# Performance work log

Measured on AMD Instinct MI355X. Metric: run time of the kernel, lower is better.

The kernel has to match this reference:

```python
import jax, jax.numpy as jnp
import numpy as np

L, B, N, D, H = 18, 2, 1024, 256, 4
DH = D // H  # head_dim = 64
LAYER_TYPES = ("self", "cross") * 9
BN_EPS = 1e-5


def setup_inputs() -> dict:
    key = jax.random.key(0)
    ks = jax.random.split(key, 8)
    s = 0.03  # small init scale keeps 18 residual layers numerically tame
    w = lambda k, shape: jax.random.normal(k, shape, jnp.float32) * s
    return dict(
        descriptors=jax.random.normal(ks[0], (B, 2, N, D), jnp.float32),
        mask=jnp.ones((B, 2, N), jnp.int32),
        qw=w(ks[1], (L, D, D)), qb=jnp.zeros((L, D), jnp.float32),
        kw=w(ks[2], (L, D, D)), kb=jnp.zeros((L, D), jnp.float32),
        vw=w(ks[3], (L, D, D)), vb=jnp.zeros((L, D), jnp.float32),
        ow=w(ks[4], (L, D, D)), ob=jnp.zeros((L, D), jnp.float32),
        w1=w(ks[5], (L, 2 * D, 2 * D)), b1=jnp.zeros((L, 2 * D), jnp.float32),
        bn_g=jnp.ones((L, 2 * D), jnp.float32), bn_b=jnp.zeros((L, 2 * D), jnp.float32),
        w2=w(ks[6], (L, 2 * D, D)), b2=jnp.zeros((L, D), jnp.float32),
    )


def _attention(x, src, m, i, qw, qb, kw, kb, vw, vb, ow, ob):
    b, n, d = x.shape
    q = (x @ qw[i] + qb[i]).reshape(b, n, H, DH)
    k = (src @ kw[i] + kb[i]).reshape(b, -1, H, DH)
    v = (src @ vw[i] + vb[i]).reshape(b, -1, H, DH)
    scores = jnp.einsum("bnhd,bmhd->bhnm", q, k) / (DH ** 0.5)
    scores = jnp.where(m[:, None, None, :] == 0, jnp.float32(-1e9), scores)
    probs = jax.nn.softmax(scores, axis=-1)  # fp32, matches torch dtype=float32
    out = jnp.einsum("bhnm,bmhd->bnhd", probs, v).reshape(b, n, d)
    return out @ ow[i] + ob[i]


def _propagate(x, src, m, i, qw, qb, kw, kb, vw, vb, ow, ob, w1, b1, bn_g, bn_b, w2, b2):
    a = _attention(x, src, m, i, qw, qb, kw, kb, vw, vb, ow, ob)
    h = jnp.concatenate([x, a], axis=-1)        # [B, N, 2D]
    h = h @ w1[i] + b1[i]                       # [B, N, 2D]
    # BatchNorm1d (training mode): per-channel stats over batch and keypoint dims
    mean = h.mean(axis=(0, 1))
    var = ((h - mean) ** 2).mean(axis=(0, 1))   # biased variance, as torch BN uses
    h = (h - mean) / jnp.sqrt(var + BN_EPS) * bn_g[i] + bn_b[i]
    h = jax.nn.relu(h)
    return h @ w2[i] + b2[i]                    # [B, N, D]


def reference(descriptors, mask, qw, qb, kw, kb, vw, vb, ow, ob, w1, b1, bn_g, bn_b, w2, b2):
    d0, d1 = descriptors[:, 0], descriptors[:, 1]
    m0, m1 = mask[:, 0], mask[:, 1]
    params = (qw, qb, kw, kb, vw, vb, ow, ob, w1, b1, bn_g, bn_b, w2, b2)
    for i, lt in enumerate(LAYER_TYPES):
        if lt == "cross":
            s0, s1, sm0, sm1 = d1, d0, m1, m0
        else:  # self
            s0, s1, sm0, sm1 = d0, d1, m0, m1
        delta0 = _propagate(d0, s0, sm0, i, *params)
        delta1 = _propagate(d1, s1, sm1, i, *params)
        d0 = d0 + delta0
        d1 = d1 + delta1
    return jnp.stack([d0, d1], axis=1)
```

## Files before the change

### kernel.cpp

```cpp
#include <hip/hip_runtime.h>


typedef __attribute__((ext_vector_type(8))) short bf16x8;
typedef __attribute__((ext_vector_type(4))) short bf16x4;
typedef __attribute__((ext_vector_type(4))) float floatx4;

__device__ __forceinline__ short f2b(float f) {
  unsigned u = __builtin_bit_cast(unsigned, f);
  unsigned r = (u + 0x7FFFu + ((u >> 16) & 1u)) >> 16;
  return (short)r;
}
__device__ __forceinline__ unsigned pack2(float a, float b) {
  return (unsigned)(unsigned short)f2b(a) | ((unsigned)(unsigned short)f2b(b) << 16);
}
__device__ __forceinline__ void split2(float a, float b, unsigned& h, unsigned& l) {
  unsigned short ha = (unsigned short)f2b(a), hb = (unsigned short)f2b(b);
  float fa = __builtin_bit_cast(float, (unsigned)ha << 16);
  float fb = __builtin_bit_cast(float, (unsigned)hb << 16);
  h = (unsigned)ha | ((unsigned)hb << 16);
  l = pack2(a - fa, b - fb);
}

__device__ __forceinline__ void gl2lds16(const void* g, void* l) {
  __builtin_amdgcn_global_load_lds(
      (const __attribute__((address_space(1))) unsigned*)g,
      (__attribute__((address_space(3))) unsigned*)l, 16, 0, 0);
}

__device__ __forceinline__ floatx4 mfma16_bf16(bf16x4 a, bf16x4 b, floatx4 c) {
#if __has_builtin(__builtin_amdgcn_mfma_f32_16x16x16_bf16)
  return __builtin_amdgcn_mfma_f32_16x16x16_bf16(a, b, c, 0, 0, 0);
#elif __has_builtin(__builtin_amdgcn_mfma_f32_16x16x16bf16_1k)
  return __builtin_amdgcn_mfma_f32_16x16x16bf16_1k(a, b, c, 0, 0, 0);
#else
  asm volatile("v_mfma_f32_16x16x16_bf16 %0, %1, %2, %0" : "+v"(c) : "v"(a), "v"(b));
  return c;
#endif
}

#define BARW   asm volatile("s_barrier" ::: "memory")
#define WAITV5 asm volatile("s_waitcnt vmcnt(5)" ::: "memory")
#define WAITV0 asm volatile("s_waitcnt vmcnt(0)" ::: "memory")

#define GEMM_IDS                                        \
  const int tid = threadIdx.x;                          \
  const int lane = tid & 63, w = tid >> 6;              \
  const int wy = w >> 1, wx = w & 1;                    \
  const int quad = lane >> 4, l16 = lane & 15;          \
  const int lr = lane >> 3;                             \
  const int lcs = (((lane & 7) ^ lr) & 7) * 8;          \
  const floatx4 z4 = {0.f, 0.f, 0.f, 0.f};

__device__ __forceinline__ void mfma_step_sw(const short* As, const short* Bs,
                                             int wy, int wx, int quad, int l16,
                                             floatx4 acc[2][4]) {
#pragma unroll
  for (int kk = 0; kk < 2; ++kk) {
    const int sw = (((kk * 4 + quad) ^ (l16 & 7)) * 8);
    bf16x8 a0 = *(const bf16x8*)&As[(wy * 32 + l16) * 64 + sw];
    bf16x8 a1 = *(const bf16x8*)&As[(wy * 32 + 16 + l16) * 64 + sw];
    bf16x8 b[4];
#pragma unroll
    for (int ni = 0; ni < 4; ++ni)
      b[ni] = *(const bf16x8*)&Bs[(wx * 64 + ni * 16 + l16) * 64 + sw];
#pragma unroll
    for (int ni = 0; ni < 4; ++ni) {
      acc[0][ni] = __builtin_amdgcn_mfma_f32_16x16x32_bf16(a0, b[ni], acc[0][ni], 0, 0, 0);
      acc[1][ni] = __builtin_amdgcn_mfma_f32_16x16x32_bf16(a1, b[ni], acc[1][ni], 0, 0, 0);
    }
  }
}

__device__ __forceinline__ void mfma_step_sw32(const short* As, const short* Bs,
                                               int wy, int wx, int quad, int l16,
                                               floatx4 acc[4]) {
#pragma unroll
  for (int kk = 0; kk < 2; ++kk) {
    const int sw = (((kk * 4 + quad) ^ (l16 & 7)) * 8);
    bf16x8 a0 = *(const bf16x8*)&As[(wy * 16 + l16) * 64 + sw];
    bf16x8 b[4];
#pragma unroll
    for (int ni = 0; ni < 4; ++ni)
      b[ni] = *(const bf16x8*)&Bs[(wx * 64 + ni * 16 + l16) * 64 + sw];
#pragma unroll
    for (int ni = 0; ni < 4; ++ni)
      acc[ni] = __builtin_amdgcn_mfma_f32_16x16x32_bf16(a0, b[ni], acc[ni], 0, 0, 0);
  }
}

__device__ __forceinline__ void mfma_step_sw32x64(const short* As, const short* Bs,
                                                  int wy, int wx, int quad, int l16,
                                                  floatx4 acc[2]) {
#pragma unroll
  for (int kk = 0; kk < 2; ++kk) {
    const int sw = (((kk * 4 + quad) ^ (l16 & 7)) * 8);
    bf16x8 a0 = *(const bf16x8*)&As[(wy * 16 + l16) * 64 + sw];
    bf16x8 b[2];
#pragma unroll
    for (int ni = 0; ni < 2; ++ni)
      b[ni] = *(const bf16x8*)&Bs[(wx * 32 + ni * 16 + l16) * 64 + sw];
#pragma unroll
    for (int ni = 0; ni < 2; ++ni)
      acc[ni] = __builtin_amdgcn_mfma_f32_16x16x32_bf16(a0, b[ni], acc[ni], 0, 0, 0);
  }
}

__global__ __launch_bounds__(256) void wfuse(
    const float* __restrict__ ow, const float* __restrict__ w1,
    short* __restrict__ wbuf) {
  __shared__ short As_h[64 * 64], As_l[64 * 64];
  __shared__ short Bs_h[128 * 64], Bs_l[128 * 64];
  const int blk = blockIdx.x;
  const int layer = blk >> 4, sub = blk & 15;
  const int kp0 = (sub & 3) * 64, n0 = (sub >> 2) * 128;
  const float* A = ow + (size_t)layer * 65536;
  const float* Bw = w1 + (size_t)layer * 262144 + 256 * 512;
  short* w1t = wbuf + (size_t)layer * 655360 + 262144;
  GEMM_IDS;
  (void)lr; (void)lcs;
  floatx4 acc[2][4] = {{z4, z4, z4, z4}, {z4, z4, z4, z4}};
  const int ar = tid >> 2, aq = tid & 3;
  const int bn = tid & 127, bkh = tid >> 7;

  for (int s = 0; s < 4; ++s) {
    const int k0 = s * 64;
    const float* Ar = &A[(size_t)(kp0 + ar) * 256 + k0 + aq * 16];
    float4 f0 = *(const float4*)&Ar[0];
    float4 f1 = *(const float4*)&Ar[4];
    float4 f2 = *(const float4*)&Ar[8];
    float4 f3 = *(const float4*)&Ar[12];
    float bv[32];
#pragma unroll
    for (int kk2 = 0; kk2 < 32; ++kk2)
      bv[kk2] = Bw[(size_t)(k0 + bkh * 32 + kk2) * 512 + n0 + bn];

    __syncthreads();
    {
      uint4 hi, lo;
      split2(f0.x, f0.y, hi.x, lo.x);
      split2(f0.z, f0.w, hi.y, lo.y);
      split2(f1.x, f1.y, hi.z, lo.z);
      split2(f1.z, f1.w, hi.w, lo.w);
      int sl = ((aq * 2) ^ (ar & 7)) * 8;
      *(uint4*)&As_h[ar * 64 + sl] = hi;
      *(uint4*)&As_l[ar * 64 + sl] = lo;
      split2(f2.x, f2.y, hi.x, lo.x);
      split2(f2.z, f2.w, hi.y, lo.y);
      split2(f3.x, f3.y, hi.z, lo.z);
      split2(f3.z, f3.w, hi.w, lo.w);
      sl = ((aq * 2 + 1) ^ (ar & 7)) * 8;
      *(uint4*)&As_h[ar * 64 + sl] = hi;
      *(uint4*)&As_l[ar * 64 + sl] = lo;
    }
#pragma unroll
    for (int cc = 0; cc < 4; ++cc) {
      uint4 hi, lo;
      split2(bv[cc * 8 + 0], bv[cc * 8 + 1], hi.x, lo.x);
      split2(bv[cc * 8 + 2], bv[cc * 8 + 3], hi.y, lo.y);
      split2(bv[cc * 8 + 4], bv[cc * 8 + 5], hi.z, lo.z);
      split2(bv[cc * 8 + 6], bv[cc * 8 + 7], hi.w, lo.w);
      int sl = ((bkh * 4 + cc) ^ (bn & 7)) * 8;
      *(uint4*)&Bs_h[bn * 64 + sl] = hi;
      *(uint4*)&Bs_l[bn * 64 + sl] = lo;
    }
    __syncthreads();
    mfma_step_sw(As_h, Bs_h, wy, wx, quad, l16, acc);
    mfma_step_sw(As_h, Bs_l, wy, wx, quad, l16, acc);
    mfma_step_sw(As_l, Bs_h, wy, wx, quad, l16, acc);
  }
#pragma unroll
  for (int mi = 0; mi < 2; ++mi)
#pragma unroll
    for (int ni = 0; ni < 4; ++ni) {
      int col = n0 + wx * 64 + ni * 16 + l16;
      int row0 = kp0 + wy * 32 + mi * 16 + quad * 4;
      uint2 uu;
      uu.x = pack2(acc[mi][ni][0], acc[mi][ni][1]);
      uu.y = pack2(acc[mi][ni][2], acc[mi][ni][3]);
      *(uint2*)&w1t[(size_t)col * 512 + 256 + row0] = uu;
    }
}

__global__ __launch_bounds__(256) void wprep(
    const float* __restrict__ qw, const float* __restrict__ kw,
    const float* __restrict__ vw, const float* __restrict__ w1,
    const float* __restrict__ w2, const float* __restrict__ ob,
    const float* __restrict__ b1, short* __restrict__ wbuf,
    float* __restrict__ beff, const float* __restrict__ desc,
    float* __restrict__ xd, short* __restrict__ xb,
    float* __restrict__ psz) {
  __shared__ float SH[64 * 65];
  int blk = blockIdx.x;
  int t = threadIdx.x;
  if (blk < 2016) {
    int layer = blk / 112;
    int sub = blk % 112;
    const float* W; int Kd, Nd, k0, n0; size_t ooff;
    if (sub < 48) {
      int wsel = sub >> 4; int tt = sub & 15;
      k0 = (tt >> 2) * 64; n0 = (tt & 3) * 64; Kd = 256; Nd = 256;
      W = (wsel == 0 ? qw : wsel == 1 ? kw : vw) + (size_t)layer * 65536;
      ooff = (size_t)wsel * 65536;
    } else if (sub < 80) {
      int tt = sub - 48; k0 = (tt >> 3) * 64; n0 = (tt & 7) * 64;
      Kd = 512; Nd = 512; W = w1 + (size_t)layer * 262144; ooff = 262144;
    } else {
      int tt = sub - 80; k0 = (tt >> 2) * 64; n0 = (tt & 3) * 64;
      Kd = 512; Nd = 256; W = w2 + (size_t)layer * 131072; ooff = 524288;
    }
    short* out = wbuf + (size_t)layer * 655360 + ooff;
    const int rr = t >> 4;
    const int c4 = (t & 15) * 4;
#pragma unroll
    for (int i = 0; i < 4; ++i) {
      float4 v = *(const float4*)&W[(size_t)(k0 + i * 16 + rr) * Nd + n0 + c4];
      float* tp = &SH[(i * 16 + rr) * 65 + c4];
      tp[0] = v.x; tp[1] = v.y; tp[2] = v.z; tp[3] = v.w;
    }
    __syncthreads();
    const int n = t >> 2;
    const int kq = t & 3;
    float v[16];
#pragma unroll
    for (int kk = 0; kk < 16; ++kk)
      v[kk] = SH[(kq * 16 + kk) * 65 + n];
    unsigned u[8];
#pragma unroll
    for (int j2 = 0; j2 < 8; ++j2) u[j2] = pack2(v[2 * j2], v[2 * j2 + 1]);
    short* op = &out[(size_t)(n0 + n) * Kd + k0 + kq * 16];
    uint4 o1; o1.x = u[0]; o1.y = u[1]; o1.z = u[2]; o1.w = u[3];
    uint4 o2; o2.x = u[4]; o2.y = u[5]; o2.z = u[6]; o2.w = u[7];
    *(uint4*)&op[0] = o1;
    *(uint4*)&op[8] = o2;
  } else if (blk < 2160) {
    int bb = blk - 2016;
    int layer = bb >> 3;
    int n0 = (bb & 7) * 64;
    const float* obL = ob + (size_t)layer * 256;
    const float* w1L = w1 + (size_t)layer * 262144 + 256 * 512;
    int n = n0 + (t & 63);
    int part = t >> 6;
    float s = 0.f;
    for (int i = part * 64; i < part * 64 + 64; ++i)
      s += obL[i] * w1L[(size_t)i * 512 + n];
    SH[part * 64 + (t & 63)] = s;
    __syncthreads();
    if (t < 64) {
      float tot = SH[t] + SH[64 + t] + SH[128 + t] + SH[192 + t] +
                  b1[(size_t)layer * 512 + n0 + t];
      beff[(size_t)layer * 512 + n0 + t] = tot;
    }
  } else if (blk < 3184) {
    int idx = (blk - 2160) * 256 + t;
    int fi = idx << 2;
    int hi = (fi >> 19) & 1;
    int lo = (fi >> 18) & 1;
    int sj = (fi & ~(3 << 18)) | (lo << 19) | (hi << 18);
    float4 v = *(const float4*)&desc[sj];
    *(float4*)&xd[fi] = v;
    uint2 uu; uu.x = pack2(v.x, v.y); uu.y = pack2(v.z, v.w);
    *(uint2*)&xb[fi] = uu;
  } else {
    int idx = (blk - 3184) * 1024 + t * 4;
    float4 zz = {0.f, 0.f, 0.f, 0.f};
    *(float4*)&psz[idx] = zz;
  }
}

__global__ __launch_bounds__(256) void gemm_qkv(
    const short* __restrict__ xb, const short* __restrict__ wbufL,
    const float* __restrict__ qb_, const float* __restrict__ kb_,
    const float* __restrict__ vb_,
    short* __restrict__ q, short* __restrict__ kout, short* __restrict__ vT,
    int cross) {
  __shared__ short SM[2 * 2048 + 2 * 8192];
  short* As = SM;
  short* Bs = SM + 4096;
  const int rb = blockIdx.x * 32;
  const int cb = blockIdx.y * 128;
  const int seg = cb >> 8;
  const int cbl = cb & 255;
  int arb = rb;
  if (seg) arb = (rb & 2047) | ((((rb >> 11) ^ cross) & 1) << 11);
  const short* A = xb + (size_t)arb * 256;
  const short* Wt = wbufL + (size_t)seg * 65536 + (size_t)cbl * 256;
  const float* bias = (seg == 0 ? qb_ : seg == 1 ? kb_ : vb_) + cbl;
  GEMM_IDS;
  floatx4 acc[4] = {z4, z4, z4, z4};

#define QKV_STAGE(s, buf)                                                          \
  {                                                                                \
    int k0 = (s) * 64;                                                             \
    gl2lds16(&A[(size_t)(w * 8 + lr) * 256 + k0 + lcs], &As[(buf) * 2048 + (w * 8) * 64]); \
    _Pragma("unroll") for (int i = 0; i < 4; ++i)                                  \
      gl2lds16(&Wt[(size_t)(i * 32 + w * 8 + lr) * 256 + k0 + lcs],                \
               &Bs[(buf) * 8192 + (i * 32 + w * 8) * 64]);                         \
  }

  QKV_STAGE(0, 0);
  QKV_STAGE(1, 1);
  for (int s = 0; s < 4; ++s) {
    int buf = s & 1;
    if (s < 3) { WAITV5; } else { WAITV0; }
    BARW;
    mfma_step_sw32(&As[buf * 2048], &Bs[buf * 8192], wy, wx, quad, l16, acc);
    BARW;
    if (s < 2) QKV_STAGE(s + 2, buf);
  }

  if (seg < 2) {
    short* C = (seg == 0 ? q : kout) + (size_t)rb * 256 + cbl;
#pragma unroll
    for (int ni = 0; ni < 4; ++ni) {
      int col = wx * 64 + ni * 16 + l16;
      float bc = bias[col];
#pragma unroll
      for (int reg = 0; reg < 4; ++reg) {
        int row = wy * 16 + quad * 4 + reg;
        C[(size_t)row * 256 + col] = f2b(acc[ni][reg] + bc);
      }
    }
  } else {
    short* T = SM + 4096 + w * 1536;
    const int sb = rb >> 10;
    const int hh = (cbl >> 6) + wx;
    const int z = sb * 4 + hh;
#pragma unroll
    for (int ni = 0; ni < 4; ++ni) {
      int col = wx * 64 + ni * 16 + l16;
      float bc = bias[col];
#pragma unroll
      for (int reg = 0; reg < 4; ++reg)
        T[(ni * 16 + l16) * 24 + quad * 4 + reg] = f2b(acc[ni][reg] + bc);
    }
    short* dst = &vT[((size_t)z * 64 + lane) * 1024 + (rb & 1023) + wy * 16];
    *(uint4*)&dst[0] = *(const uint4*)&T[lane * 24 + 0];
    *(uint4*)&dst[8] = *(const uint4*)&T[lane * 24 + 8];
  }
#undef QKV_STAGE
}

__global__ __launch_bounds__(256) void attn_mfma(
    const short* __restrict__ q, const short* __restrict__ k,
    const short* __restrict__ vT, const int* __restrict__ mask,
    short* __restrict__ attnb, int cross) {
  __shared__ short Ks[2][2][4096];
  __shared__ short Vs[2][2][4096];
  const int tid = threadIdx.x;
  const int lane = tid & 63, w = tid >> 6;
  const int wv = w & 1, wq = w >> 1;
  const int quad = lane >> 4, l16 = lane & 15;
  const int lr = lane >> 3;
  const int lcs = (((lane & 7) ^ lr) & 7) * 8;
  const int qt = blockIdx.x;
  const int z = blockIdx.y;
  const int sb = z >> 2, h = z & 3;
  const int s = sb >> 1, b = sb & 1;
  const int rowbase = sb * 1024;
  const int* mp = mask + (b * 2 + (s ^ cross)) * 1024;

  const int qrow = qt * 32 + wq * 16 + l16;
  bf16x8 qf[2];
#pragma unroll
  for (int kk = 0; kk < 2; ++kk)
    qf[kk] = *(const bf16x8*)&q[(size_t)(rowbase + qrow) * 256 + h * 64 + kk * 32 + quad * 8];

  const floatx4 z4 = {0.f, 0.f, 0.f, 0.f};
  floatx4 o4[4] = {z4, z4, z4, z4};
  float mrun = -1e30f, lsum = 0.f;

#define ATT_STAGE(t, buf)                                                               \
  {                                                                                     \
    int key0s = wv * 512 + (t) * 64;                                                    \
    _Pragma("unroll") for (int j = 0; j < 4; ++j) {                                     \
      gl2lds16(&k[(size_t)(rowbase + key0s + j * 16 + wq * 8 + lr) * 256 + h * 64 + lcs], \
               &Ks[buf][wv][(j * 16 + wq * 8) * 64]);                                   \
      gl2lds16(&vT[((size_t)z * 64 + j * 16 + wq * 8 + lr) * 1024 + key0s + lcs],       \
               &Vs[buf][wv][(j * 16 + wq * 8) * 64]);                                   \
    }                                                                                   \
  }

  ATT_STAGE(0, 0);
  __syncthreads();
  for (int t = 0; t < 8; ++t) {
    int buf = t & 1;
    if (t < 7) ATT_STAGE(t + 1, buf ^ 1);
    const int key0 = wv * 512 + t * 64;

    floatx4 sA[4] = {z4, z4, z4, z4};
#pragma unroll
    for (int kk = 0; kk < 2; ++kk) {
      const int sw = (((kk * 4 + quad) ^ (l16 & 7)) * 8);
#pragma unroll
      for (int mt = 0; mt < 4; ++mt) {
        bf16x8 kf = *(const bf16x8*)&Ks[buf][wv][(mt * 16 + l16) * 64 + sw];
        sA[mt] = __builtin_amdgcn_mfma_f32_16x16x32_bf16(kf, qf[kk], sA[mt], 0, 0, 0);
      }
    }
    float scv[4][4];
    float tmax = -1e30f;
#pragma unroll
    for (int mt = 0; mt < 4; ++mt) {
      int4 mv = *(const int4*)&mp[key0 + mt * 16 + quad * 4];
      scv[mt][0] = sA[mt][0] * 0.125f + (mv.x == 0 ? -1.0e9f : 0.f);
      scv[mt][1] = sA[mt][1] * 0.125f + (mv.y == 0 ? -1.0e9f : 0.f);
      scv[mt][2] = sA[mt][2] * 0.125f + (mv.z == 0 ? -1.0e9f : 0.f);
      scv[mt][3] = sA[mt][3] * 0.125f + (mv.w == 0 ? -1.0e9f : 0.f);
#pragma unroll
      for (int reg = 0; reg < 4; ++reg) tmax = fmaxf(tmax, scv[mt][reg]);
    }
    tmax = fmaxf(tmax, __shfl_xor(tmax, 16));
    tmax = fmaxf(tmax, __shfl_xor(tmax, 32));
    float mnew = fmaxf(mrun, tmax);
    float corr = __expf(mrun - mnew);
    mrun = mnew;
    lsum *= corr;
#pragma unroll
    for (int dt = 0; dt < 4; ++dt)
#pragma unroll
      for (int reg = 0; reg < 4; ++reg) o4[dt][reg] *= corr;

    bf16x4 pb[4];
#pragma unroll
    for (int mt = 0; mt < 4; ++mt) {
      float e0 = __expf(scv[mt][0] - mnew);
      float e1 = __expf(scv[mt][1] - mnew);
      float e2 = __expf(scv[mt][2] - mnew);
      float e3 = __expf(scv[mt][3] - mnew);
      lsum += (e0 + e1) + (e2 + e3);
      union { bf16x4 v; uint2 u; } pu;
      pu.u.x = pack2(e0, e1); pu.u.y = pack2(e2, e3);
      pb[mt] = pu.v;
    }
#pragma unroll
    for (int mt = 0; mt < 4; ++mt) {
      const int c2 = mt * 2 + (quad >> 1);
      const int sub = (quad & 1) * 4;
#pragma unroll
      for (int dt = 0; dt < 4; ++dt) {
        bf16x4 vf = *(const bf16x4*)&Vs[buf][wv][(dt * 16 + l16) * 64 +
                                                 ((c2 ^ (l16 & 7)) * 8) + sub];
        o4[dt] = mfma16_bf16(vf, pb[mt], o4[dt]);
      }
    }
    __syncthreads();
  }
  lsum += __shfl_xor(lsum, 16);
  lsum += __shfl_xor(lsum, 32);

  float* MG = (float*)&Ks[0][0][0];
  const int mo = (wq * 64 + lane) * 18;
  if (wv == 1) {
    MG[mo] = mrun;
    MG[mo + 1] = lsum;
#pragma unroll
    for (int dt = 0; dt < 4; ++dt)
#pragma unroll
      for (int reg = 0; reg < 4; ++reg) MG[mo + 2 + dt * 4 + reg] = o4[dt][reg];
  }
  __syncthreads();
  if (wv == 0) {
    float m2 = MG[mo], l2 = MG[mo + 1];
    float mm = fmaxf(mrun, m2);
    float ca = __expf(mrun - mm), cb2 = __expf(m2 - mm);
    float inv = 1.f / (ca * lsum + cb2 * l2);
    short* op = &attnb[(size_t)(rowbase + qrow) * 256 + h * 64 + quad * 4];
#pragma unroll
    for (int dt = 0; dt < 4; ++dt) {
      float v0 = (ca * o4[dt][0] + cb2 * MG[mo + 2 + dt * 4 + 0]) * inv;
      float v1 = (ca * o4[dt][1] + cb2 * MG[mo + 2 + dt * 4 + 1]) * inv;
      float v2 = (ca * o4[dt][2] + cb2 * MG[mo + 2 + dt * 4 + 2]) * inv;
      float v3 = (ca * o4[dt][3] + cb2 * MG[mo + 2 + dt * 4 + 3]) * inv;
      uint2 uu;
      uu.x = pack2(v0, v1);
      uu.y = pack2(v2, v3);
      *(uint2*)&op[dt * 16] = uu;
    }
  }
#undef ATT_STAGE
}

__global__ __launch_bounds__(256) void gemm_w1(
    const short* __restrict__ xb, const short* __restrict__ attnb,
    const short* __restrict__ w1t, const float* __restrict__ beff,
    float* __restrict__ hbuf, float* __restrict__ psumL, float* __restrict__ psqL) {
  __shared__ short SM[2 * 2048 + 2 * 8192];
  __shared__ float Ps[2][2][128];
  short* As = SM;
  short* Bs = SM + 4096;
  const int rb = blockIdx.x * 32, cb = blockIdx.y * 128;
  const int str = rb >> 11;
  GEMM_IDS;
  floatx4 acc[4] = {z4, z4, z4, z4};

#define W1_STAGE(s, buf)                                                            \
  {                                                                                 \
    int k0 = (s) * 64;                                                              \
    const short* Ap = ((s) < 4 ? xb : attnb) + (size_t)rb * 256;                    \
    int kb = k0 & 255;                                                              \
    gl2lds16(&Ap[(size_t)(w * 8 + lr) * 256 + kb + lcs], &As[(buf) * 2048 + (w * 8) * 64]); \
    _Pragma("unroll") for (int i = 0; i < 4; ++i)                                   \
      gl2lds16(&w1t[(size_t)(cb + i * 32 + w * 8 + lr) * 512 + k0 + lcs],           \
               &Bs[(buf) * 8192 + (i * 32 + w * 8) * 64]);                          \
  }

  W1_STAGE(0, 0);
  W1_STAGE(1, 1);
  for (int s = 0; s < 8; ++s) {
    int buf = s & 1;
    if (s < 7) { WAITV5; } else { WAITV0; }
    BARW;
    mfma_step_sw32(&As[buf * 2048], &Bs[buf * 8192], wy, wx, quad, l16, acc);
    BARW;
    if (s < 6) W1_STAGE(s + 2, buf);
  }
  float colsum[4], colsq[4];
#pragma unroll
  for (int ni = 0; ni < 4; ++ni) { colsum[ni] = 0.f; colsq[ni] = 0.f; }
#pragma unroll
  for (int ni = 0; ni < 4; ++ni) {
    int col = wx * 64 + ni * 16 + l16;
    float bc = beff[cb + col];
#pragma unroll
    for (int reg = 0; reg < 4; ++reg) {
      int row = rb + wy * 16 + quad * 4 + reg;
      float val = acc[ni][reg] + bc;
      hbuf[(size_t)row * 512 + cb + col] = val;
      colsum[ni] += val; colsq[ni] += val * val;
    }
  }
#pragma unroll
  for (int ni = 0; ni < 4; ++ni)
#pragma unroll
    for (int d = 16; d < 64; d <<= 1) {
      colsum[ni] += __shfl_xor(colsum[ni], d);
      colsq[ni]  += __shfl_xor(colsq[ni], d);
    }
  if (quad == 0) {
#pragma unroll
    for (int ni = 0; ni < 4; ++ni) {
      Ps[wy][0][wx * 64 + ni * 16 + l16] = colsum[ni];
      Ps[wy][1][wx * 64 + ni * 16 + l16] = colsq[ni];
    }
  }
  __syncthreads();
  if (tid < 128) {
    atomicAdd(&psumL[str * 512 + cb + tid], Ps[0][0][tid] + Ps[1][0][tid]);
    atomicAdd(&psqL [str * 512 + cb + tid], Ps[0][1][tid] + Ps[1][1][tid]);
  }
#undef W1_STAGE
}

__global__ __launch_bounds__(256) void gemm_w2(
    const float* __restrict__ hbuf, const short* __restrict__ w2t,
    const float* __restrict__ b2_, const float* __restrict__ psumL,
    const float* __restrict__ psqL, const float* __restrict__ g,
    const float* __restrict__ be, float* __restrict__ xd, short* __restrict__ xb,
    float* __restrict__ outp) {
  __shared__ short SM[2 * 2048 + 2 * 4096];
  __shared__ float s_scale[512], s_shift[512];
  short* As = SM;
  short* Bs = SM + 4096;
  const int rb = blockIdx.x * 32, cb = blockIdx.y * 64;
  const int str = rb >> 11;
  GEMM_IDS;
  floatx4 acc[2] = {z4, z4};
#pragma unroll
  for (int cc = 0; cc < 2; ++cc) {
    int c = tid + cc * 256;
    float sum = psumL[str * 512 + c];
    float sq  = psqL [str * 512 + c];
    float mean = sum * (1.f / 2048.f);
    float var = sq * (1.f / 2048.f) - mean * mean;
    float rstd = rsqrtf(var + 1e-5f);
    float gs = g[c] * rstd;
    s_scale[c] = gs;
    s_shift[c] = be[c] - mean * gs;
  }
  __syncthreads();

  const int p = tid & 7, ar = tid >> 3;

#define W2_STAGE_A(s, buf)                                                         \
  {                                                                                \
    int k0 = (s) * 64;                                                             \
    int cs = k0 + ((p ^ (ar & 7)) * 8);                                            \
    float4 h0 = *(const float4*)&hbuf[(size_t)(rb + ar) * 512 + cs];               \
    float4 h1 = *(const float4*)&hbuf[(size_t)(rb + ar) * 512 + cs + 4];           \
    float4 sc0 = *(const float4*)&s_scale[cs];                                     \
    float4 sc1 = *(const float4*)&s_scale[cs + 4];                                 \
    float4 sh0 = *(const float4*)&s_shift[cs];                                     \
    float4 sh1 = *(const float4*)&s_shift[cs + 4];                                 \
    uint4 pk;                                                                      \
    pk.x = pack2(fmaxf(h0.x * sc0.x + sh0.x, 0.f), fmaxf(h0.y * sc0.y + sh0.y, 0.f)); \
    pk.y = pack2(fmaxf(h0.z * sc0.z + sh0.z, 0.f), fmaxf(h0.w * sc0.w + sh0.w, 0.f)); \
    pk.z = pack2(fmaxf(h1.x * sc1.x + sh1.x, 0.f), fmaxf(h1.y * sc1.y + sh1.y, 0.f)); \
    pk.w = pack2(fmaxf(h1.z * sc1.z + sh1.z, 0.f), fmaxf(h1.w * sc1.w + sh1.w, 0.f)); \
    *(uint4*)&As[(buf) * 2048 + ar * 64 + p * 8] = pk;                             \
  }
#define W2_STAGE_B(s, buf)                                                         \
  {                                                                                \
    int k0 = (s) * 64;                                                             \
    _Pragma("unroll") for (int i = 0; i < 2; ++i)                                  \
      gl2lds16(&w2t[(size_t)(cb + i * 32 + w * 8 + lr) * 512 + k0 + lcs],          \
               &Bs[(buf) * 4096 + (i * 32 + w * 8) * 64]);                         \
  }

  W2_STAGE_A(0, 0);
  W2_STAGE_B(0, 0);
  __syncthreads();
  for (int s = 0; s < 8; ++s) {
    int buf = s & 1;
    if (s < 7) W2_STAGE_B(s + 1, buf ^ 1);
    mfma_step_sw32x64(&As[buf * 2048], &Bs[buf * 4096], wy, wx, quad, l16, acc);
    if (s < 7) W2_STAGE_A(s + 1, buf ^ 1);
    __syncthreads();
  }
#pragma unroll
  for (int ni = 0; ni < 2; ++ni) {
    int col = cb + wx * 32 + ni * 16 + l16;
    float bc = b2_[col];
#pragma unroll
    for (int reg = 0; reg < 4; ++reg) {
      int row = rb + wy * 16 + quad * 4 + reg;
      float r = xd[(size_t)row * 256 + col] + acc[ni][reg] + bc;
      xd[(size_t)row * 256 + col] = r;
      xb[(size_t)row * 256 + col] = f2b(r);
      if (outp) {
        int ss = row >> 11, bb = (row >> 10) & 1, n = row & 1023;
        outp[(size_t)((bb * 2 + ss) * 1024 + n) * 256 + col] = r;
      }
    }
  }
#undef W2_STAGE_A
#undef W2_STAGE_B
}

extern "C" void kernel_launch(void* const* d_in, const int* in_sizes, int n_in,
                              void* d_out, int out_size, void* d_ws, size_t ws_size,
                              hipStream_t stream) {
  (void)in_sizes; (void)n_in; (void)out_size; (void)ws_size;
  const float* desc = (const float*)d_in[0];
  const int*   mask = (const int*)d_in[1];
  const float* qw = (const float*)d_in[2];
  const float* qb = (const float*)d_in[3];
  const float* kw = (const float*)d_in[4];
  const float* kb = (const float*)d_in[5];
  const float* vw = (const float*)d_in[6];
  const float* vb = (const float*)d_in[7];
  const float* ow = (const float*)d_in[8];
  const float* ob = (const float*)d_in[9];
  const float* w1 = (const float*)d_in[10];
  const float* b1 = (const float*)d_in[11];
  const float* bn_g = (const float*)d_in[12];
  const float* bn_b = (const float*)d_in[13];
  const float* w2 = (const float*)d_in[14];
  const float* b2 = (const float*)d_in[15];
  float* out = (float*)d_out;

  char* base = (char*)d_ws;
  float* xd    = (float*)(base);
  float* hbuf  = (float*)(base + (4u << 20));
  short* xb    = (short*)(base + (12u << 20));
  short* qb16  = (short*)(base + (14u << 20));
  short* kb16  = (short*)(base + (16u << 20));
  short* vTb   = (short*)(base + (18u << 20));
  short* attnb = (short*)(base + (20u << 20));
  float* psum  = (float*)(base + (22u << 20));
  float* psq   = psum + 18 * 1024;
  float* beff  = psq + 18 * 1024;
  short* wbuf  = (short*)(base + (24u << 20));

  wprep<<<3220, 256, 0, stream>>>(qw, kw, vw, w1, w2, ob, b1,
                                  wbuf, beff, desc, xd, xb, psum);
  wfuse<<<288, 256, 0, stream>>>(ow, w1, wbuf);

  for (int i = 0; i < 18; ++i) {
    int cross = i & 1;
    short* wb = wbuf + (size_t)i * 655360;

    gemm_qkv<<<dim3(128, 6), 256, 0, stream>>>(
        xb, wb, qb + (size_t)i * 256, kb + (size_t)i * 256, vb + (size_t)i * 256,
        qb16, kb16, vTb, cross);
    attn_mfma<<<dim3(32, 16), 256, 0, stream>>>(qb16, kb16, vTb, mask, attnb, cross);
    gemm_w1<<<dim3(128, 4), 256, 0, stream>>>(xb, attnb, wb + 262144,
                                              beff + (size_t)i * 512,
                                              hbuf, psum + (size_t)i * 1024,
                                              psq + (size_t)i * 1024);
    gemm_w2<<<dim3(128, 4), 256, 0, stream>>>(hbuf, wb + 524288,
                                              b2 + (size_t)i * 256,
                                              psum + (size_t)i * 1024,
                                              psq + (size_t)i * 1024,
                                              bn_g + (size_t)i * 512,
                                              bn_b + (size_t)i * 512, xd, xb,
                                              (i == 17) ? out : nullptr);
  }
}
```

Baseline: 958.4 us.

## Retile weight prep, cache mask in LDS, and software-pipeline attention and W2 loads

```diff
diff --git a/kernel.cpp b/kernel.cpp
--- a/kernel.cpp
+++ b/kernel.cpp
@@ -39,8 +39,11 @@
 }
 
 #define BARW   asm volatile("s_barrier" ::: "memory")
+#define WAITV8 asm volatile("s_waitcnt vmcnt(8)" ::: "memory")
 #define WAITV5 asm volatile("s_waitcnt vmcnt(5)" ::: "memory")
+#define WAITV4 asm volatile("s_waitcnt vmcnt(4)" ::: "memory")
 #define WAITV0 asm volatile("s_waitcnt vmcnt(0)" ::: "memory")
+#define LGKM0  asm volatile("s_waitcnt lgkmcnt(0)" ::: "memory")
 
 #define GEMM_IDS                                        \
   const int tid = threadIdx.x;                          \
@@ -189,51 +192,54 @@
     float* __restrict__ beff, const float* __restrict__ desc,
     float* __restrict__ xd, short* __restrict__ xb,
     float* __restrict__ psz) {
-  __shared__ float SH[64 * 65];
+  __shared__ float SH[64 * 130];
   int blk = blockIdx.x;
   int t = threadIdx.x;
-  if (blk < 2016) {
-    int layer = blk / 112;
-    int sub = blk % 112;
+  if (blk < 1296) {
+    int layer = blk / 72;
+    int sub = blk % 72;
     const float* W; int Kd, Nd, k0, n0; size_t ooff;
-    if (sub < 48) {
-      int wsel = sub >> 4; int tt = sub & 15;
-      k0 = (tt >> 2) * 64; n0 = (tt & 3) * 64; Kd = 256; Nd = 256;
+    if (sub < 24) {
+      int wsel = sub / 8; int tt = sub & 7;
+      k0 = (tt >> 1) * 64; n0 = (tt & 1) * 128; Kd = 256; Nd = 256;
       W = (wsel == 0 ? qw : wsel == 1 ? kw : vw) + (size_t)layer * 65536;
       ooff = (size_t)wsel * 65536;
-    } else if (sub < 80) {
-      int tt = sub - 48; k0 = (tt >> 3) * 64; n0 = (tt & 7) * 64;
+    } else if (sub < 56) {
+      int tt = sub - 24; k0 = (tt >> 2) * 64; n0 = (tt & 3) * 128;
       Kd = 512; Nd = 512; W = w1 + (size_t)layer * 262144; ooff = 262144;
     } else {
-      int tt = sub - 80; k0 = (tt >> 2) * 64; n0 = (tt & 3) * 64;
+      int tt = sub - 56; k0 = (tt >> 1) * 64; n0 = (tt & 1) * 128;
       Kd = 512; Nd = 256; W = w2 + (size_t)layer * 131072; ooff = 524288;
     }
     short* out = wbuf + (size_t)layer * 655360 + ooff;
     const int rr = t >> 4;
     const int c4 = (t & 15) * 4;
 #pragma unroll
-    for (int i = 0; i < 4; ++i) {
-      float4 v = *(const float4*)&W[(size_t)(k0 + i * 16 + rr) * Nd + n0 + c4];
-      float* tp = &SH[(i * 16 + rr) * 65 + c4];
-      tp[0] = v.x; tp[1] = v.y; tp[2] = v.z; tp[3] = v.w;
-    }
+    for (int i = 0; i < 4; ++i)
+#pragma unroll
+      for (int hf = 0; hf < 2; ++hf) {
+        float4 v = *(const float4*)&W[(size_t)(k0 + i * 16 + rr) * Nd + n0 + hf * 64 + c4];
+        float* tp = &SH[(i * 16 + rr) * 130 + hf * 64 + c4];
+        tp[0] = v.x; tp[1] = v.y; tp[2] = v.z; tp[3] = v.w;
+      }
     __syncthreads();
-    const int n = t >> 2;
-    const int kq = t & 3;
-    float v[16];
-#pragma unroll
-    for (int kk = 0; kk < 16; ++kk)
-      v[kk] = SH[(kq * 16 + kk) * 65 + n];
-    unsigned u[8];
-#pragma unroll
-    for (int j2 = 0; j2 < 8; ++j2) u[j2] = pack2(v[2 * j2], v[2 * j2 + 1]);
-    short* op = &out[(size_t)(n0 + n) * Kd + k0 + kq * 16];
-    uint4 o1; o1.x = u[0]; o1.y = u[1]; o1.z = u[2]; o1.w = u[3];
-    uint4 o2; o2.x = u[4]; o2.y = u[5]; o2.z = u[6]; o2.w = u[7];
-    *(uint4*)&op[0] = o1;
-    *(uint4*)&op[8] = o2;
-  } else if (blk < 2160) {
-    int bb = blk - 2016;
+    const int n = t >> 1;
+    const int kh = (t & 1) * 32;
+    float v[32];
+#pragma unroll
+    for (int kk = 0; kk < 32; ++kk)
+      v[kk] = SH[(kh + kk) * 130 + n];
+    unsigned u[16];
+#pragma unroll
+    for (int j2 = 0; j2 < 16; ++j2) u[j2] = pack2(v[2 * j2], v[2 * j2 + 1]);
+    short* op = &out[(size_t)(n0 + n) * Kd + k0 + kh];
+#pragma unroll
+    for (int q4 = 0; q4 < 4; ++q4) {
+      uint4 o; o.x = u[q4 * 4]; o.y = u[q4 * 4 + 1]; o.z = u[q4 * 4 + 2]; o.w = u[q4 * 4 + 3];
+      *(uint4*)&op[q4 * 8] = o;
+    }
+  } else if (blk < 1440) {
+    int bb = blk - 1296;
     int layer = bb >> 3;
     int n0 = (bb & 7) * 64;
     const float* obL = ob + (size_t)layer * 256;
@@ -250,8 +256,8 @@
                   b1[(size_t)layer * 512 + n0 + t];
       beff[(size_t)layer * 512 + n0 + t] = tot;
     }
-  } else if (blk < 3184) {
-    int idx = (blk - 2160) * 256 + t;
+  } else if (blk < 2464) {
+    int idx = (blk - 1440) * 256 + t;
     int fi = idx << 2;
     int hi = (fi >> 19) & 1;
     int lo = (fi >> 18) & 1;
@@ -261,7 +267,7 @@
     uint2 uu; uu.x = pack2(v.x, v.y); uu.y = pack2(v.z, v.w);
     *(uint2*)&xb[fi] = uu;
   } else {
-    int idx = (blk - 3184) * 1024 + t * 4;
+    int idx = (blk - 2464) * 1024 + t * 4;
     float4 zz = {0.f, 0.f, 0.f, 0.f};
     *(float4*)&psz[idx] = zz;
   }
@@ -346,6 +352,7 @@
     short* __restrict__ attnb, int cross) {
   __shared__ short Ks[2][2][4096];
   __shared__ short Vs[2][2][4096];
+  __shared__ float Msk[1024];
   const int tid = threadIdx.x;
   const int lane = tid & 63, w = tid >> 6;
   const int wv = w & 1, wq = w >> 1;
@@ -365,6 +372,14 @@
   for (int kk = 0; kk < 2; ++kk)
     qf[kk] = *(const bf16x8*)&q[(size_t)(rowbase + qrow) * 256 + h * 64 + kk * 32 + quad * 8];
 
+  {
+    int4 mv = *(const int4*)&mp[tid * 4];
+    Msk[tid * 4 + 0] = (mv.x == 0) ? -1.0e9f : 0.f;
+    Msk[tid * 4 + 1] = (mv.y == 0) ? -1.0e9f : 0.f;
+    Msk[tid * 4 + 2] = (mv.z == 0) ? -1.0e9f : 0.f;
+    Msk[tid * 4 + 3] = (mv.w == 0) ? -1.0e9f : 0.f;
+  }
+
   const floatx4 z4 = {0.f, 0.f, 0.f, 0.f};
   floatx4 o4[4] = {z4, z4, z4, z4};
   float mrun = -1e30f, lsum = 0.f;
@@ -384,10 +399,12 @@
   __syncthreads();
   for (int t = 0; t < 8; ++t) {
     int buf = t & 1;
-    if (t < 7) ATT_STAGE(t + 1, buf ^ 1);
+    if (t < 7) { ATT_STAGE(t + 1, buf ^ 1); WAITV8; } else { WAITV0; }
+    BARW;
     const int key0 = wv * 512 + t * 64;
 
     floatx4 sA[4] = {z4, z4, z4, z4};
+    __builtin_amdgcn_s_setprio(1);
 #pragma unroll
     for (int kk = 0; kk < 2; ++kk) {
       const int sw = (((kk * 4 + quad) ^ (l16 & 7)) * 8);
@@ -397,15 +414,16 @@
         sA[mt] = __builtin_amdgcn_mfma_f32_16x16x32_bf16(kf, qf[kk], sA[mt], 0, 0, 0);
       }
     }
+    __builtin_amdgcn_s_setprio(0);
     float scv[4][4];
     float tmax = -1e30f;
 #pragma unroll
     for (int mt = 0; mt < 4; ++mt) {
-      int4 mv = *(const int4*)&mp[key0 + mt * 16 + quad * 4];
-      scv[mt][0] = sA[mt][0] * 0.125f + (mv.x == 0 ? -1.0e9f : 0.f);
-      scv[mt][1] = sA[mt][1] * 0.125f + (mv.y == 0 ? -1.0e9f : 0.f);
-      scv[mt][2] = sA[mt][2] * 0.125f + (mv.z == 0 ? -1.0e9f : 0.f);
-      scv[mt][3] = sA[mt][3] * 0.125f + (mv.w == 0 ? -1.0e9f : 0.f);
+      float4 mk = *(const float4*)&Msk[key0 + mt * 16 + quad * 4];
+      scv[mt][0] = sA[mt][0] * 0.125f + mk.x;
+      scv[mt][1] = sA[mt][1] * 0.125f + mk.y;
+      scv[mt][2] = sA[mt][2] * 0.125f + mk.z;
+      scv[mt][3] = sA[mt][3] * 0.125f + mk.w;
 #pragma unroll
       for (int reg = 0; reg < 4; ++reg) tmax = fmaxf(tmax, scv[mt][reg]);
     }
@@ -432,6 +450,7 @@
       pu.u.x = pack2(e0, e1); pu.u.y = pack2(e2, e3);
       pb[mt] = pu.v;
     }
+    __builtin_amdgcn_s_setprio(1);
 #pragma unroll
     for (int mt = 0; mt < 4; ++mt) {
       const int c2 = mt * 2 + (quad >> 1);
@@ -443,7 +462,9 @@
         o4[dt] = mfma16_bf16(vf, pb[mt], o4[dt]);
       }
     }
-    __syncthreads();
+    __builtin_amdgcn_s_setprio(0);
+    LGKM0;
+    BARW;
   }
   lsum += __shfl_xor(lsum, 16);
   lsum += __shfl_xor(lsum, 32);
@@ -580,22 +601,28 @@
   __syncthreads();
 
   const int p = tid & 7, ar = tid >> 3;
-
-#define W2_STAGE_A(s, buf)                                                         \
+  float4 ra0, ra1;
+
+#define W2_A_LOAD(s)                                                               \
+  {                                                                               \
+    int k0 = (s) * 64;                                                            \
+    int cs = k0 + ((p ^ (ar & 7)) * 8);                                           \
+    ra0 = *(const float4*)&hbuf[(size_t)(rb + ar) * 512 + cs];                    \
+    ra1 = *(const float4*)&hbuf[(size_t)(rb + ar) * 512 + cs + 4];                \
+  }
+#define W2_A_WRITE(s, buf)                                                         \
   {                                                                                \
     int k0 = (s) * 64;                                                             \
     int cs = k0 + ((p ^ (ar & 7)) * 8);                                            \
-    float4 h0 = *(const float4*)&hbuf[(size_t)(rb + ar) * 512 + cs];               \
-    float4 h1 = *(const float4*)&hbuf[(size_t)(rb + ar) * 512 + cs + 4];           \
     float4 sc0 = *(const float4*)&s_scale[cs];                                     \
     float4 sc1 = *(const float4*)&s_scale[cs + 4];                                 \
     float4 sh0 = *(const float4*)&s_shift[cs];                                     \
     float4 sh1 = *(const float4*)&s_shift[cs + 4];                                 \
     uint4 pk;                                                                      \
-    pk.x = pack2(fmaxf(h0.x * sc0.x + sh0.x, 0.f), fmaxf(h0.y * sc0.y + sh0.y, 0.f)); \
-    pk.y = pack2(fmaxf(h0.z * sc0.z + sh0.z, 0.f), fmaxf(h0.w * sc0.w + sh0.w, 0.f)); \
-    pk.z = pack2(fmaxf(h1.x * sc1.x + sh1.x, 0.f), fmaxf(h1.y * sc1.y + sh1.y, 0.f)); \
-    pk.w = pack2(fmaxf(h1.z * sc1.z + sh1.z, 0.f), fmaxf(h1.w * sc1.w + sh1.w, 0.f)); \
+    pk.x = pack2(fmaxf(ra0.x * sc0.x + sh0.x, 0.f), fmaxf(ra0.y * sc0.y + sh0.y, 0.f)); \
+    pk.y = pack2(fmaxf(ra0.z * sc0.z + sh0.z, 0.f), fmaxf(ra0.w * sc0.w + sh0.w, 0.f)); \
+    pk.z = pack2(fmaxf(ra1.x * sc1.x + sh1.x, 0.f), fmaxf(ra1.y * sc1.y + sh1.y, 0.f)); \
+    pk.w = pack2(fmaxf(ra1.z * sc1.z + sh1.z, 0.f), fmaxf(ra1.w * sc1.w + sh1.w, 0.f)); \
     *(uint4*)&As[(buf) * 2048 + ar * 64 + p * 8] = pk;                             \
   }
 #define W2_STAGE_B(s, buf)                                                         \
@@ -606,15 +633,18 @@
                &Bs[(buf) * 4096 + (i * 32 + w * 8) * 64]);                         \
   }
 
-  W2_STAGE_A(0, 0);
+  W2_A_LOAD(0);
   W2_STAGE_B(0, 0);
-  __syncthreads();
+  W2_A_WRITE(0, 0);
+  LGKM0;
   for (int s = 0; s < 8; ++s) {
     int buf = s & 1;
-    if (s < 7) W2_STAGE_B(s + 1, buf ^ 1);
+    if (s < 7) { W2_A_LOAD(s + 1); W2_STAGE_B(s + 1, buf ^ 1); WAITV4; } else { WAITV0; }
+    BARW;
     mfma_step_sw32x64(&As[buf * 2048], &Bs[buf * 4096], wy, wx, quad, l16, acc);
-    if (s < 7) W2_STAGE_A(s + 1, buf ^ 1);
-    __syncthreads();
+    if (s < 7) W2_A_WRITE(s + 1, buf ^ 1);
+    LGKM0;
+    BARW;
   }
 #pragma unroll
   for (int ni = 0; ni < 2; ++ni) {
@@ -632,7 +662,8 @@
       }
     }
   }
-#undef W2_STAGE_A
+#undef W2_A_LOAD
+#undef W2_A_WRITE
 #undef W2_STAGE_B
 }
 
@@ -671,7 +702,7 @@
   float* beff  = psq + 18 * 1024;
   short* wbuf  = (short*)(base + (24u << 20));
 
-  wprep<<<3220, 256, 0, stream>>>(qw, kw, vw, w1, w2, ob, b1,
+  wprep<<<2500, 256, 0, stream>>>(qw, kw, vw, w1, w2, ob, b1,
                                   wbuf, beff, desc, xd, xb, psum);
   wfuse<<<288, 256, 0, stream>>>(ow, w1, wbuf);
 
```

New measurement: 930.8 us. 2.9% less time.
